# Optimization experiments

Measured on AMD Instinct MI355X. Metric: run time of the kernel, lower is better.

## Reference

```python
import jax, jax.numpy as jnp
import numpy as np

BLOCK = 64
SCALING = 64 / 64  # alpha / block_size


def setup_inputs() -> dict:
    key = jax.random.key(0)
    ks = jax.random.split(key, 5)
    B, N, DIN, DOUT = 2, 2048, 4096, 4096
    nb_in, nb_out = DIN // BLOCK, DOUT // BLOCK
    return {
        "x": jax.random.normal(ks[0], (B, N, DIN), dtype=jnp.float32),
        "W_base": jax.random.normal(ks[1], (DOUT, DIN), dtype=jnp.float32) * 0.02,
        "b_base": jax.random.normal(ks[2], (DOUT,), dtype=jnp.float32),
        "U": jax.random.normal(ks[3], (BLOCK, nb_in, nb_out), dtype=jnp.float32) / BLOCK,
        "V": jax.random.normal(ks[4], (nb_out, BLOCK, BLOCK), dtype=jnp.float32) * 0.02,
        "S": jnp.ones((1,), dtype=jnp.float32),
    }


def reference(x, W_base, b_base, U, V, S):
    B, N, DIN = x.shape
    DOUT = W_base.shape[0]
    nb_in = U.shape[1]  # in_features // block_size
    # base linear: y = x @ W^T + b
    result = jnp.einsum("bnd,od->bno", x, W_base) + b_base
    # block-structured adapter path
    xr = x.reshape(B, N, nb_in, BLOCK)            # [b, n, in_blocks, block]
    t = jnp.einsum("bnid,dio->bnod", xr, U)       # mix across input blocks per lane d
    t = jnp.einsum("bnod,ode->bnoe", t, V)        # mix within each output block
    scaling = SCALING * S[0]
    result = result + scaling * t.reshape(B, N, DOUT)
    return result
```

## Files before the change

### kernel.cpp

```cpp
#include <hip/hip_runtime.h>


typedef __attribute__((ext_vector_type(4))) float float4v;
typedef __attribute__((ext_vector_type(4))) int   int4v;

#define K_TOT 4096
#define M_TOT 4096
#define N_TOT 4096

__global__ void trans_uv(const float* __restrict__ U, const float* __restrict__ V,
                         float* __restrict__ Ut, float* __restrict__ Vt) {
  int idx = blockIdx.x * 256 + threadIdx.x;
  if (idx < 262144) {
    int d = idx & 63, o = (idx >> 6) & 63, i = idx >> 12;
    Ut[idx] = U[(d * 64 + i) * 64 + o];
  } else {
    int j = idx - 262144;
    int d = j & 63, e = (j >> 6) & 63, o = j >> 12;
    Vt[j] = V[(o * 64 + d) * 64 + e];
  }
}

__global__ __launch_bounds__(1024) void quant_rows(
    const float* __restrict__ W, const float* __restrict__ Ut,
    const float* __restrict__ Vt, const float* __restrict__ Sp,
    const float* __restrict__ X, char* __restrict__ Wq, char* __restrict__ Xq,
    float* __restrict__ sw, float* __restrict__ sx) {
  __shared__ float red[16];
  const int row = blockIdx.x;
  const int t = threadIdx.x;
  const float s = Sp[0];
  float4v v;
  if (row < 4096) {
    const int o = row >> 6, e = row & 63;
    const int i = t >> 4, d0 = (t & 15) << 2;
    const float4v wv = *(const float4v*)(W + (size_t)row * 4096 + t * 4);
    const float4v u4 = *(const float4v*)(Ut + (i * 64 + o) * 64 + d0);
    const float4v v4 = *(const float4v*)(Vt + (o * 64 + e) * 64 + d0);
#pragma unroll
    for (int j = 0; j < 4; ++j) v[j] = wv[j] + s * u4[j] * v4[j];
  } else {
    v = *(const float4v*)(X + (size_t)(row - 4096) * 4096 + t * 4);
  }
  float m = fmaxf(fmaxf(fabsf(v[0]), fabsf(v[1])),
                  fmaxf(fabsf(v[2]), fabsf(v[3])));
#pragma unroll
  for (int off = 32; off; off >>= 1) m = fmaxf(m, __shfl_xor(m, off));
  if ((t & 63) == 0) red[t >> 6] = m;
  __syncthreads();
  if (t < 16) {
    float mm = red[t];
#pragma unroll
    for (int off = 8; off; off >>= 1) mm = fmaxf(mm, __shfl_xor(mm, off));
    if (t == 0) red[0] = mm;
  }
  __syncthreads();
  const float mx = red[0];
  const float inv = mx > 0.f ? 127.f / mx : 0.f;
  int q[4];
#pragma unroll
  for (int j = 0; j < 4; ++j) {
    int qi = __float2int_rn(v[j] * inv);
    q[j] = qi > 127 ? 127 : (qi < -127 ? -127 : qi);
  }
  const int packed = (q[0] & 0xff) | ((q[1] & 0xff) << 8) |
                     ((q[2] & 0xff) << 16) | (q[3] << 24);
  if (row < 4096) {
    ((int*)Wq)[(size_t)row * 1024 + t] = packed;
    if (t == 0) sw[row] = mx * (1.f / 127.f);
  } else {
    ((int*)Xq)[(size_t)(row - 4096) * 1024 + t] = packed;
    if (t == 0) sx[row - 4096] = mx * (1.f / 127.f);
  }
}

#define GL16(g, l)                                                    \
  __builtin_amdgcn_global_load_lds(                                   \
      (__attribute__((address_space(1))) void*)(g),                   \
      (__attribute__((address_space(3))) void*)(l), 16, 0, 0)

#define BARRIER() asm volatile("s_barrier" ::: "memory")
#define VMC6() asm volatile("s_waitcnt vmcnt(6)" ::: "memory")
#define VMC0() asm volatile("s_waitcnt vmcnt(0)" ::: "memory")
#define VMNONE()

__global__ __launch_bounds__(512, 2) void gemm256(
    const char* __restrict__ A,
    const char* __restrict__ Bq,
    const float* __restrict__ bias,
    const float* __restrict__ sx,
    const float* __restrict__ sw,
    float* __restrict__ C) {
  __shared__ char lds[2][2][2][16384];

  const int tid = threadIdx.x;
  const int w = tid >> 6;
  const int l = tid & 63;
  const int l15 = l & 15;
  const int hi = l >> 4;

  int b = blockIdx.x;
  b = (b & 7) * 32 + (b >> 3);
  const int brow = (b >> 4) * 256;
  const int bcol = (b & 15) * 256;

  const int wr = w >> 2;
  const int wc = w & 3;
  const int wcH = wc >> 1, wcL = wc & 1;

  const int b2 = (l15 >> 2) & 1;
  const int cx = hi ^ (l15 & 3);
  const int rdK0 = (((b2 ^ 0) << 2) | cx) << 4;
  const int rdK1 = (((b2 ^ 1) << 2) | cx) << 4;
  const int rowOff = l15 << 7;

  const int rowL = l >> 3;
  const int cL = (l & 7) ^ rowL;
  const char* pa = A + (size_t)(brow + w * 8 + rowL) * 4096 + cL * 16;
  const char* pb = Bq + (size_t)(bcol + w * 8 + rowL) * 4096 + cL * 16;
  const int ldsC0 = w * 1024;
  const int ldsC1 = 8192 + w * 1024;

#define STAGE(gp, BUF, OP, H, kt)                                           \
  do {                                                                      \
    GL16((gp) + (size_t)(H) * (128 * 4096) + (kt), &lds[BUF][OP][H][ldsC0]);\
    GL16((gp) + (size_t)(H) * (128 * 4096) + (64 * 4096) + (kt),            \
         &lds[BUF][OP][H][ldsC1]);                                          \
  } while (0)

  int4v acc[8][4];
#pragma unroll
  for (int m = 0; m < 8; ++m)
#pragma unroll
    for (int j = 0; j < 4; ++j) acc[m][j] = (int4v){0, 0, 0, 0};
  int4v af[4][2];
  int4v bfr[4][2];

#define READ_A(BUF, MB)                                                     \
  _Pragma("unroll") for (int mm = 0; mm < 4; ++mm) {                        \
    const char* ap = &lds[BUF][0][wr][((MB) + mm) * 2048 + rowOff];         \
    af[mm][0] = *(const int4v*)&ap[rdK0];                                   \
    af[mm][1] = *(const int4v*)&ap[rdK1];                                   \
  }

#define READ_B(BUF, NH)                                                     \
  _Pragma("unroll") for (int jj = 0; jj < 2; ++jj) {                        \
    const char* bp =                                                        \
        &lds[BUF][1][wcH][((wcL)*64 + (NH)*32 + jj * 16) * 128 + rowOff];   \
    bfr[(NH)*2 + jj][0] = *(const int4v*)&bp[rdK0];                         \
    bfr[(NH)*2 + jj][1] = *(const int4v*)&bp[rdK1];                         \
  }

#define MFMA16(MB, NB)                                                      \
  do {                                                                      \
    __builtin_amdgcn_s_setprio(1);                                          \
    _Pragma("unroll") for (int mm = 0; mm < 4; ++mm)                        \
        _Pragma("unroll") for (int nn = 0; nn < 2; ++nn) {                  \
      acc[(MB) + mm][(NB) + nn] = __builtin_amdgcn_mfma_i32_16x16x64_i8(    \
          af[mm][0], bfr[(NB) + nn][0], acc[(MB) + mm][(NB) + nn], 0, 0, 0);\
      acc[(MB) + mm][(NB) + nn] = __builtin_amdgcn_mfma_i32_16x16x64_i8(    \
          af[mm][1], bfr[(NB) + nn][1], acc[(MB) + mm][(NB) + nn], 0, 0, 0);\
    }                                                                       \
    __builtin_amdgcn_s_setprio(0);                                          \
  } while (0)

#define TILE(BUF, TT, DA1, DB, DA0, VM)                                    \
  do {                                                                     \
    READ_A(BUF, 0); READ_B(BUF, 0);                                        \
    if (DA1) STAGE(pa, 1 - (BUF), 0, 1, ((TT) + 1) * 128);                 \
    BARRIER(); MFMA16(0, 0);                                               \
    READ_B(BUF, 1);                                                        \
    BARRIER(); MFMA16(0, 2);                                               \
    READ_A(BUF, 4);                                                        \
    if (DB) STAGE(pb, BUF, 1, 0, ((TT) + 2) * 128);                        \
    BARRIER(); MFMA16(4, 0);                                               \
    if (DB) STAGE(pb, BUF, 1, 1, ((TT) + 2) * 128);                        \
    if (DA0) STAGE(pa, BUF, 0, 0, ((TT) + 2) * 128);                       \
    VM();                                                                  \
    BARRIER(); MFMA16(4, 2);                                               \
  } while (0)

  STAGE(pa, 0, 0, 0, 0);
  STAGE(pa, 0, 0, 1, 0);
  STAGE(pb, 0, 1, 0, 0);
  STAGE(pb, 0, 1, 1, 0);
  STAGE(pb, 1, 1, 0, 128);
  STAGE(pb, 1, 1, 1, 128);
  STAGE(pa, 1, 0, 0, 128);
  VMC6();
  BARRIER();

  for (int t = 0; t < 30; t += 2) {
    TILE(0, t, 1, 1, 1, VMC6);
    TILE(1, t + 1, 1, 1, 1, VMC6);
  }
  TILE(0, 30, 1, 0, 0, VMC0);
  TILE(1, 31, 0, 0, 0, VMNONE);

  const int r0 = brow + wr * 128 + (l >> 4) * 4;
  const int c0 = bcol + wc * 64;
  float sxr[8][4];
#pragma unroll
  for (int m = 0; m < 8; ++m)
#pragma unroll
    for (int v = 0; v < 4; ++v) sxr[m][v] = sx[r0 + m * 16 + v];
#pragma unroll
  for (int j = 0; j < 4; ++j) {
    const int col = c0 + j * 16 + l15;
    const float bv = bias[col];
    const float swc = sw[col];
#pragma unroll
    for (int m = 0; m < 8; ++m) {
      const int row = r0 + m * 16;
#pragma unroll
      for (int v = 0; v < 4; ++v)
        C[(size_t)(row + v) * N_TOT + col] =
            (float)acc[m][j][v] * (sxr[m][v] * swc) + bv;
    }
  }
}

extern "C" void kernel_launch(void* const* d_in, const int* in_sizes, int n_in,
                              void* d_out, int out_size, void* d_ws, size_t ws_size,
                              hipStream_t stream) {
  const float* x = (const float*)d_in[0];
  const float* Wb = (const float*)d_in[1];
  const float* bb = (const float*)d_in[2];
  const float* U = (const float*)d_in[3];
  const float* V = (const float*)d_in[4];
  const float* S = (const float*)d_in[5];
  float* out = (float*)d_out;

  char* Wq = (char*)d_ws;
  char* Xq = Wq + (size_t)4096 * 4096;
  float* sw = (float*)(Xq + (size_t)4096 * 4096);
  float* sx = sw + 4096;
  float* Ut = (float*)d_out;
  float* Vt = Ut + 262144;

  trans_uv<<<2048, 256, 0, stream>>>(U, V, Ut, Vt);
  quant_rows<<<8192, 1024, 0, stream>>>(Wb, Ut, Vt, S, x, Wq, Xq, sw, sx);

  gemm256<<<256, 512, 0, stream>>>(Xq, Wq, bb, sx, sw, out);
}
```

Measured before the change: 102.1 us.

## Simplify GEMM main loop to two barriers per tile with batched staging

```diff
diff --git a/kernel.cpp b/kernel.cpp
--- a/kernel.cpp
+++ b/kernel.cpp
@@ -80,9 +80,8 @@
       (__attribute__((address_space(3))) void*)(l), 16, 0, 0)
 
 #define BARRIER() asm volatile("s_barrier" ::: "memory")
-#define VMC6() asm volatile("s_waitcnt vmcnt(6)" ::: "memory")
+#define VMC8() asm volatile("s_waitcnt vmcnt(8)" ::: "memory")
 #define VMC0() asm volatile("s_waitcnt vmcnt(0)" ::: "memory")
-#define VMNONE()
 
 __global__ __launch_bounds__(512, 2) void gemm256(
     const char* __restrict__ A,
@@ -164,38 +163,42 @@
     __builtin_amdgcn_s_setprio(0);                                          \
   } while (0)
 
-#define TILE(BUF, TT, DA1, DB, DA0, VM)                                    \
+#define TILE(BUF, TT, DOS, VM)                                             \
   do {                                                                     \
-    READ_A(BUF, 0); READ_B(BUF, 0);                                        \
-    if (DA1) STAGE(pa, 1 - (BUF), 0, 1, ((TT) + 1) * 128);                 \
-    BARRIER(); MFMA16(0, 0);                                               \
+    VM();                                                                  \
+    BARRIER();                                                             \
+    READ_A(BUF, 0);                                                        \
+    READ_B(BUF, 0);                                                        \
     READ_B(BUF, 1);                                                        \
-    BARRIER(); MFMA16(0, 2);                                               \
+    MFMA16(0, 0);                                                          \
+    MFMA16(0, 2);                                                          \
     READ_A(BUF, 4);                                                        \
-    if (DB) STAGE(pb, BUF, 1, 0, ((TT) + 2) * 128);                        \
-    BARRIER(); MFMA16(4, 0);                                               \
-    if (DB) STAGE(pb, BUF, 1, 1, ((TT) + 2) * 128);                        \
-    if (DA0) STAGE(pa, BUF, 0, 0, ((TT) + 2) * 128);                       \
-    VM();                                                                  \
-    BARRIER(); MFMA16(4, 2);                                               \
+    MFMA16(4, 0);                                                          \
+    MFMA16(4, 2);                                                          \
+    BARRIER();                                                             \
+    if (DOS) {                                                             \
+      STAGE(pa, BUF, 0, 0, ((TT) + 2) * 128);                              \
+      STAGE(pa, BUF, 0, 1, ((TT) + 2) * 128);                              \
+      STAGE(pb, BUF, 1, 0, ((TT) + 2) * 128);                              \
+      STAGE(pb, BUF, 1, 1, ((TT) + 2) * 128);                              \
+    }                                                                      \
   } while (0)
 
   STAGE(pa, 0, 0, 0, 0);
   STAGE(pa, 0, 0, 1, 0);
   STAGE(pb, 0, 1, 0, 0);
   STAGE(pb, 0, 1, 1, 0);
+  STAGE(pa, 1, 0, 0, 128);
+  STAGE(pa, 1, 0, 1, 128);
   STAGE(pb, 1, 1, 0, 128);
   STAGE(pb, 1, 1, 1, 128);
-  STAGE(pa, 1, 0, 0, 128);
-  VMC6();
-  BARRIER();
 
   for (int t = 0; t < 30; t += 2) {
-    TILE(0, t, 1, 1, 1, VMC6);
-    TILE(1, t + 1, 1, 1, 1, VMC6);
-  }
-  TILE(0, 30, 1, 0, 0, VMC0);
-  TILE(1, 31, 0, 0, 0, VMNONE);
+    TILE(0, t, 1, VMC8);
+    TILE(1, t + 1, 1, VMC8);
+  }
+  TILE(0, 30, 0, VMC8);
+  TILE(1, 31, 0, VMC0);
 
   const int r0 = brow + wr * 128 + (l >> 4) * 4;
   const int c0 = bcol + wc * 64;
```

New measurement: 105.7 us. 3.6% more time.

## Shrink int8 GEMM block tile from 256x256 to 128x128 with four waves

Applied to the files above, without the earlier changes.

```diff
diff --git a/kernel.cpp b/kernel.cpp
--- a/kernel.cpp
+++ b/kernel.cpp
@@ -80,18 +80,18 @@
       (__attribute__((address_space(3))) void*)(l), 16, 0, 0)
 
 #define BARRIER() asm volatile("s_barrier" ::: "memory")
-#define VMC6() asm volatile("s_waitcnt vmcnt(6)" ::: "memory")
+#define VMC4() asm volatile("s_waitcnt vmcnt(4)" ::: "memory")
 #define VMC0() asm volatile("s_waitcnt vmcnt(0)" ::: "memory")
 #define VMNONE()
 
-__global__ __launch_bounds__(512, 2) void gemm256(
+__global__ __launch_bounds__(256, 2) void gemm128(
     const char* __restrict__ A,
     const char* __restrict__ Bq,
     const float* __restrict__ bias,
     const float* __restrict__ sx,
     const float* __restrict__ sw,
     float* __restrict__ C) {
-  __shared__ char lds[2][2][2][16384];
+  __shared__ char lds[2][2][2][8192];
 
   const int tid = threadIdx.x;
   const int w = tid >> 6;
@@ -100,13 +100,12 @@
   const int hi = l >> 4;
 
   int b = blockIdx.x;
-  b = (b & 7) * 32 + (b >> 3);
-  const int brow = (b >> 4) * 256;
-  const int bcol = (b & 15) * 256;
-
-  const int wr = w >> 2;
-  const int wc = w & 3;
-  const int wcH = wc >> 1, wcL = wc & 1;
+  b = (b & 7) * 128 + (b >> 3);
+  const int brow = (b >> 5) * 128;
+  const int bcol = (b & 31) * 128;
+
+  const int wr = w >> 1;
+  const int wc = w & 1;
 
   const int b2 = (l15 >> 2) & 1;
   const int cx = hi ^ (l15 & 3);
@@ -119,65 +118,62 @@
   const char* pa = A + (size_t)(brow + w * 8 + rowL) * 4096 + cL * 16;
   const char* pb = Bq + (size_t)(bcol + w * 8 + rowL) * 4096 + cL * 16;
   const int ldsC0 = w * 1024;
-  const int ldsC1 = 8192 + w * 1024;
+  const int ldsC1 = 4096 + w * 1024;
 
 #define STAGE(gp, BUF, OP, H, kt)                                           \
   do {                                                                      \
-    GL16((gp) + (size_t)(H) * (128 * 4096) + (kt), &lds[BUF][OP][H][ldsC0]);\
-    GL16((gp) + (size_t)(H) * (128 * 4096) + (64 * 4096) + (kt),            \
+    GL16((gp) + (size_t)(H) * (64 * 4096) + (kt), &lds[BUF][OP][H][ldsC0]); \
+    GL16((gp) + (size_t)(H) * (64 * 4096) + (32 * 4096) + (kt),             \
          &lds[BUF][OP][H][ldsC1]);                                          \
   } while (0)
 
-  int4v acc[8][4];
-#pragma unroll
-  for (int m = 0; m < 8; ++m)
+  int4v acc[4][4];
+#pragma unroll
+  for (int m = 0; m < 4; ++m)
 #pragma unroll
     for (int j = 0; j < 4; ++j) acc[m][j] = (int4v){0, 0, 0, 0};
   int4v af[4][2];
   int4v bfr[4][2];
 
-#define READ_A(BUF, MB)                                                     \
+#define READ_A(BUF)                                                         \
   _Pragma("unroll") for (int mm = 0; mm < 4; ++mm) {                        \
-    const char* ap = &lds[BUF][0][wr][((MB) + mm) * 2048 + rowOff];         \
+    const char* ap = &lds[BUF][0][wr][mm * 2048 + rowOff];                  \
     af[mm][0] = *(const int4v*)&ap[rdK0];                                   \
     af[mm][1] = *(const int4v*)&ap[rdK1];                                   \
   }
 
 #define READ_B(BUF, NH)                                                     \
   _Pragma("unroll") for (int jj = 0; jj < 2; ++jj) {                        \
-    const char* bp =                                                        \
-        &lds[BUF][1][wcH][((wcL)*64 + (NH)*32 + jj * 16) * 128 + rowOff];   \
+    const char* bp = &lds[BUF][1][wc][((NH)*32 + jj * 16) * 128 + rowOff];  \
     bfr[(NH)*2 + jj][0] = *(const int4v*)&bp[rdK0];                         \
     bfr[(NH)*2 + jj][1] = *(const int4v*)&bp[rdK1];                         \
   }
 
-#define MFMA16(MB, NB)                                                      \
+#define MFMA8(NB)                                                           \
   do {                                                                      \
     __builtin_amdgcn_s_setprio(1);                                          \
-    _Pragma("unroll") for (int mm = 0; mm < 4; ++mm)                        \
-        _Pragma("unroll") for (int nn = 0; nn < 2; ++nn) {                  \
-      acc[(MB) + mm][(NB) + nn] = __builtin_amdgcn_mfma_i32_16x16x64_i8(    \
-          af[mm][0], bfr[(NB) + nn][0], acc[(MB) + mm][(NB) + nn], 0, 0, 0);\
-      acc[(MB) + mm][(NB) + nn] = __builtin_amdgcn_mfma_i32_16x16x64_i8(    \
-          af[mm][1], bfr[(NB) + nn][1], acc[(MB) + mm][(NB) + nn], 0, 0, 0);\
+    _Pragma("unroll") for (int mm = 0; mm < 4; ++mm) {                      \
+      acc[mm][NB] = __builtin_amdgcn_mfma_i32_16x16x64_i8(                  \
+          af[mm][0], bfr[NB][0], acc[mm][NB], 0, 0, 0);                     \
+      acc[mm][NB] = __builtin_amdgcn_mfma_i32_16x16x64_i8(                  \
+          af[mm][1], bfr[NB][1], acc[mm][NB], 0, 0, 0);                     \
     }                                                                       \
     __builtin_amdgcn_s_setprio(0);                                          \
   } while (0)
 
-#define TILE(BUF, TT, DA1, DB, DA0, VM)                                    \
+#define TILE(BUF, TT, DA, DB, VM)                                          \
   do {                                                                     \
-    READ_A(BUF, 0); READ_B(BUF, 0);                                        \
-    if (DA1) STAGE(pa, 1 - (BUF), 0, 1, ((TT) + 1) * 128);                 \
-    BARRIER(); MFMA16(0, 0);                                               \
+    READ_A(BUF); READ_B(BUF, 0);                                           \
+    if (DA) STAGE(pa, 1 - (BUF), 0, 0, ((TT) + 1) * 128);                  \
+    BARRIER(); MFMA8(0);                                                   \
     READ_B(BUF, 1);                                                        \
-    BARRIER(); MFMA16(0, 2);                                               \
-    READ_A(BUF, 4);                                                        \
+    if (DA) STAGE(pa, 1 - (BUF), 0, 1, ((TT) + 1) * 128);                  \
+    BARRIER(); MFMA8(1);                                                   \
     if (DB) STAGE(pb, BUF, 1, 0, ((TT) + 2) * 128);                        \
-    BARRIER(); MFMA16(4, 0);                                               \
+    BARRIER(); MFMA8(2);                                                   \
     if (DB) STAGE(pb, BUF, 1, 1, ((TT) + 2) * 128);                        \
-    if (DA0) STAGE(pa, BUF, 0, 0, ((TT) + 2) * 128);                       \
     VM();                                                                  \
-    BARRIER(); MFMA16(4, 2);                                               \
+    BARRIER(); MFMA8(3);                                                   \
   } while (0)
 
   STAGE(pa, 0, 0, 0, 0);
@@ -186,22 +182,21 @@
   STAGE(pb, 0, 1, 1, 0);
   STAGE(pb, 1, 1, 0, 128);
   STAGE(pb, 1, 1, 1, 128);
-  STAGE(pa, 1, 0, 0, 128);
-  VMC6();
+  VMC4();
   BARRIER();
 
   for (int t = 0; t < 30; t += 2) {
-    TILE(0, t, 1, 1, 1, VMC6);
-    TILE(1, t + 1, 1, 1, 1, VMC6);
-  }
-  TILE(0, 30, 1, 0, 0, VMC0);
-  TILE(1, 31, 0, 0, 0, VMNONE);
-
-  const int r0 = brow + wr * 128 + (l >> 4) * 4;
+    TILE(0, t, 1, 1, VMC4);
+    TILE(1, t + 1, 1, 1, VMC4);
+  }
+  TILE(0, 30, 1, 0, VMC0);
+  TILE(1, 31, 0, 0, VMNONE);
+
+  const int r0 = brow + wr * 64 + (l >> 4) * 4;
   const int c0 = bcol + wc * 64;
-  float sxr[8][4];
-#pragma unroll
-  for (int m = 0; m < 8; ++m)
+  float sxr[4][4];
+#pragma unroll
+  for (int m = 0; m < 4; ++m)
 #pragma unroll
     for (int v = 0; v < 4; ++v) sxr[m][v] = sx[r0 + m * 16 + v];
 #pragma unroll
@@ -210,7 +205,7 @@
     const float bv = bias[col];
     const float swc = sw[col];
 #pragma unroll
-    for (int m = 0; m < 8; ++m) {
+    for (int m = 0; m < 4; ++m) {
       const int row = r0 + m * 16;
 #pragma unroll
       for (int v = 0; v < 4; ++v)
@@ -241,5 +236,5 @@
   trans_uv<<<2048, 256, 0, stream>>>(U, V, Ut, Vt);
   quant_rows<<<8192, 1024, 0, stream>>>(Wb, Ut, Vt, S, x, Wq, Xq, sw, sx);
 
-  gemm256<<<256, 512, 0, stream>>>(Xq, Wq, bb, sx, sw, out);
-}
+  gemm128<<<1024, 256, 0, stream>>>(Xq, Wq, bb, sx, sw, out);
+}
```

After: 124.4 us. 1.22x slower.
